# Kernel optimization log

Hardware: AMD Instinct MI355X
Metric: run time of the kernel (lower is better)

Reference implementation:

```python
import jax, jax.numpy as jnp
import numpy as np

N = 50000   # nodes
E = 800000  # edges
R = 2000    # relations
F = 128     # node_F / rel_F
DEPTH = 2
FD = F * (DEPTH + 1)  # 384
P = 64      # proxy rows
EPS = 1e-12


def setup_inputs() -> dict:
    key = jax.random.key(0)
    ks = jax.random.split(key, 16)
    inp = {
        'ent_emb': jax.random.normal(ks[0], (N, F), jnp.float32) * 0.05,
        'rel_emb': jax.random.normal(ks[1], (R, F), jnp.float32) * 0.05,
        'edge_src': jax.random.randint(ks[2], (E,), 0, N, jnp.int32),
        'edge_dst': jax.random.randint(ks[3], (E,), 0, N, jnp.int32),
        'edge_rel': jax.random.randint(ks[4], (E,), 0, R, jnp.int32),
        'attn_e': jax.random.normal(ks[5], (DEPTH, F, 1), jnp.float32) * 0.1,
        'gate_e': jax.random.normal(ks[6], (FD, FD), jnp.float32) * 0.05,
        'proxy_e': jax.random.normal(ks[7], (P, FD), jnp.float32) * 0.1,
        'bias_e': jnp.zeros((1, FD), jnp.float32),
        'attn_r': jax.random.normal(ks[8], (DEPTH, F, 1), jnp.float32) * 0.1,
        'gate_r': jax.random.normal(ks[9], (FD, FD), jnp.float32) * 0.05,
        'proxy_r': jax.random.normal(ks[10], (P, FD), jnp.float32) * 0.1,
        'bias_r': jnp.zeros((1, FD), jnp.float32),
    }
    return inp


def _l2norm(x, axis=-1):
    n = jnp.sqrt(jnp.sum(x * x, axis=axis, keepdims=True))
    return x / jnp.maximum(n, EPS)


def _dual(features, rel_emb, edge_src, edge_dst, edge_rel,
          attn_kernels, gate_kernel, proxy, bias):
    feats = jnp.tanh(features)            # [N, F]
    outs = [feats]
    for l in range(DEPTH):
        # per-edge relation feature (mean over relation set == gather here), L2-normalized
        rels_sum = _l2norm(rel_emb[edge_rel])          # [E, F]
        neighs = feats[edge_src]                       # [E, F]
        # Householder reflection of neighbor features across relation direction
        dot = jnp.sum(neighs * rels_sum, axis=1, keepdims=True)
        neighs = neighs - 2.0 * dot * rels_sum
        # edge_softmax normalized by dst
        att1 = jnp.squeeze(rels_sum @ attn_kernels[l], -1)   # [E]
        seg_max = jax.ops.segment_max(att1, edge_dst, num_segments=N)
        ex = jnp.exp(att1 - seg_max[edge_dst])
        seg_sum = jax.ops.segment_sum(ex, edge_dst, num_segments=N)
        att = ex / seg_sum[edge_dst]
        # weighted scatter-sum aggregation
        agg = jax.ops.segment_sum(neighs * att[:, None], edge_dst, num_segments=N)
        feats = jnp.tanh(agg)
        outs.append(feats)
    outputs = jnp.concatenate(outs, axis=1)            # [N, FD]
    proxy_att = jax.nn.softmax(_l2norm(outputs) @ _l2norm(proxy).T, axis=-1)  # [N, P]
    proxy_feature = outputs - proxy_att @ proxy
    gate = jax.nn.sigmoid(proxy_feature @ gate_kernel + bias)
    return gate * outputs + (1.0 - gate) * proxy_feature


def reference(ent_emb, rel_emb, edge_src, edge_dst, edge_rel,
              attn_e, gate_e, proxy_e, bias_e,
              attn_r, gate_r, proxy_r, bias_r):
    # initial features: mean of neighbor entity / relation embeddings per dst node
    deg = jax.ops.segment_sum(jnp.ones((E,), jnp.float32), edge_dst, num_segments=N)
    deg = jnp.maximum(deg, 1.0)[:, None]
    ent_feature = jax.ops.segment_sum(ent_emb[edge_src], edge_dst, num_segments=N) / deg
    rel_feature = jax.ops.segment_sum(rel_emb[edge_rel], edge_dst, num_segments=N) / deg
    out_ent = _dual(ent_feature, rel_emb, edge_src, edge_dst, edge_rel,
                    attn_e, gate_e, proxy_e, bias_e)
    out_rel = _dual(rel_feature, rel_emb, edge_src, edge_dst, edge_rel,
                    attn_r, gate_r, proxy_r, bias_r)
    return jnp.concatenate((out_ent, out_rel), axis=-1)  # [N, 2*FD]
```

## Files before the change

### kernel.cpp

```cpp
#include <hip/hip_runtime.h>
#include <math.h>


#define NN    50000
#define NE    800000
#define NR    2000
#define FF    128
#define FDIM  384
#define OD    768
#define PP    64
#define NEPS  1e-12f
#define NPB   32
#define FSTR  388
#define ASTR  68
#define NBLK  49

typedef unsigned int u32;
typedef unsigned short u16;
typedef __attribute__((ext_vector_type(8))) short bf16x8;
typedef __attribute__((ext_vector_type(4))) float f32x4;

__device__ int   g_rowptr[NN + 1];
__device__ int   g_cnt[NN];
__device__ int   g_bsum[64];
__device__ u32   g_csr[NE];
__device__ float g_relnorm[NR * FF];
__device__ float2 g_ew[2 * NR];
__device__ __attribute__((aligned(16))) u16 g_wt_hi[2 * FDIM * FDIM];
__device__ __attribute__((aligned(16))) u16 g_wt_lo[2 * FDIM * FDIM];
__device__ __attribute__((aligned(16))) u16 g_pxn_hi[2 * PP * FDIM];
__device__ __attribute__((aligned(16))) u16 g_pxn_lo[2 * PP * FDIM];
__device__ __attribute__((aligned(16))) u16 g_pxT_hi[2 * FDIM * PP];
__device__ __attribute__((aligned(16))) u16 g_pxT_lo[2 * FDIM * PP];

__device__ __forceinline__ float wsum64(float v) {
#pragma unroll
    for (int m = 32; m > 0; m >>= 1) v += __shfl_xor(v, m, 64);
    return v;
}
__device__ __forceinline__ float wmax64(float v) {
#pragma unroll
    for (int m = 32; m > 0; m >>= 1) v = fmaxf(v, __shfl_xor(v, m, 64));
    return v;
}
__device__ __forceinline__ void red16x2(float& a, float& b) {
#pragma unroll
    for (int m = 1; m < 16; m <<= 1) {
        float ta = __shfl_xor(a, m, 64);
        float tb = __shfl_xor(b, m, 64);
        a += ta; b += tb;
    }
}
__device__ __forceinline__ void xgr4(float4& v) {
#pragma unroll
    for (int mk = 16; mk < 64; mk <<= 1) {
        v.x += __shfl_xor(v.x, mk, 64);
        v.y += __shfl_xor(v.y, mk, 64);
        v.z += __shfl_xor(v.z, mk, 64);
        v.w += __shfl_xor(v.w, mk, 64);
    }
}
__device__ __forceinline__ void xgr1(float& v) {
#pragma unroll
    for (int mk = 16; mk < 64; mk <<= 1) v += __shfl_xor(v, mk, 64);
}

__device__ __forceinline__ u32 pack_bf(float f) {
    u32 x = __float_as_uint(f);
    u32 hr = (x + 0x7FFFu + ((x >> 16) & 1u)) & 0xFFFF0000u;
    float res = f - __uint_as_float(hr);
    u32 y = __float_as_uint(res);
    u32 lr = (y + 0x7FFFu + ((y >> 16) & 1u)) >> 16;
    return hr | lr;
}
__device__ __forceinline__ float unpack_bf(u32 pk) {
    return __uint_as_float(pk & 0xFFFF0000u) + __uint_as_float(pk << 16);
}

__device__ __forceinline__ void load_afrag(const u32* p, bf16x8& ah, bf16x8& al) {
    u32 q[8];
    *reinterpret_cast<float4*>(q)     = *reinterpret_cast<const float4*>(p);
    *reinterpret_cast<float4*>(q + 4) = *reinterpret_cast<const float4*>(p + 4);
    union { u32 u[4]; bf16x8 v; } H, L;
#pragma unroll
    for (int j = 0; j < 4; j++) {
        H.u[j] = __builtin_amdgcn_perm(q[2 * j + 1], q[2 * j], 0x07060302u);
        L.u[j] = __builtin_amdgcn_perm(q[2 * j + 1], q[2 * j], 0x05040100u);
    }
    ah = H.v; al = L.v;
}

__global__ __launch_bounds__(256) void k_zero() {
    int i = blockIdx.x * 256 + threadIdx.x;
    if (i < NN) g_cnt[i] = 0;
}

__global__ __launch_bounds__(256) void k_prep_rel(
    const float* __restrict__ rel_emb, const float* __restrict__ attn_e,
    const float* __restrict__ attn_r) {
    int wave = threadIdx.x >> 6, lane = threadIdx.x & 63;
    int r = blockIdx.x * 4 + wave;
    if (r >= NR) return;
    float2 v = *(const float2*)(rel_emb + r * FF + 2 * lane);
    float ss = wsum64(v.x * v.x + v.y * v.y);
    float inv = 1.f / fmaxf(sqrtf(ss), NEPS);
    float rn0 = v.x * inv, rn1 = v.y * inv;
    *(float2*)(g_relnorm + r * FF + 2 * lane) = make_float2(rn0, rn1);
#pragma unroll
    for (int t = 0; t < 4; t++) {
        const float* av = ((t < 2) ? attn_e : attn_r) + (t & 1) * FF + 2 * lane;
        float d = wsum64(rn0 * av[0] + rn1 * av[1]);
        if (lane == 0) ((float*)&g_ew[(t & 1) * NR + r])[t >> 1] = expf(d);
    }
}

__global__ __launch_bounds__(256) void k_prep_proxy(
    const float* __restrict__ proxy_e, const float* __restrict__ proxy_r) {
    int wave = threadIdx.x >> 6, lane = threadIdx.x & 63;
    int row = blockIdx.x * 4 + wave;
    if (row >= 2 * PP) return;
    int d = row >> 6, p = row & 63;
    const float* pr = ((d == 0) ? proxy_e : proxy_r) + p * FDIM;
    float v[6];
    float ss = 0.f;
#pragma unroll
    for (int j = 0; j < 6; j++) {
        v[j] = pr[lane + 64 * j];
        ss += v[j] * v[j];
    }
    ss = wsum64(ss);
    float inv = 1.f / fmaxf(sqrtf(ss), NEPS);
#pragma unroll
    for (int j = 0; j < 6; j++) {
        int k = lane + 64 * j;
        u32 pn = pack_bf(v[j] * inv);
        g_pxn_hi[(d * PP + p) * FDIM + k] = (u16)(pn >> 16);
        g_pxn_lo[(d * PP + p) * FDIM + k] = (u16)(pn & 0xFFFFu);
        u32 pt = pack_bf(v[j]);
        g_pxT_hi[(d * FDIM + k) * PP + p] = (u16)(pt >> 16);
        g_pxT_lo[(d * FDIM + k) * PP + p] = (u16)(pt & 0xFFFFu);
    }
}

__global__ __launch_bounds__(256) void k_prep_wt(
    const float* __restrict__ gate_e, const float* __restrict__ gate_r) {
    int idx = blockIdx.x * 256 + threadIdx.x;
    if (idx >= 2 * FDIM * FDIM) return;
    int d = idx / (FDIM * FDIM);
    int rem = idx - d * (FDIM * FDIM);
    int k = rem / FDIM;
    int f = rem - k * FDIM;
    float wv = (d ? gate_r : gate_e)[k * FDIM + f];
    u32 pk = pack_bf(wv);
    g_wt_hi[(d * FDIM + f) * FDIM + k] = (u16)(pk >> 16);
    g_wt_lo[(d * FDIM + f) * FDIM + k] = (u16)(pk & 0xFFFFu);
}

__global__ __launch_bounds__(256) void k_count(const int* __restrict__ dst) {
    int e = blockIdx.x * 256 + threadIdx.x;
    if (e < NE) atomicAdd(&g_cnt[dst[e]], 1);
}

__global__ __launch_bounds__(1024) void k_scan1() {
    __shared__ int s[1024];
    int b = blockIdx.x, tid = threadIdx.x;
    int i = b * 1024 + tid;
    int v = (i < NN) ? g_cnt[i] : 0;
    s[tid] = v;
    __syncthreads();
    for (int off = 1; off < 1024; off <<= 1) {
        int t = (tid >= off) ? s[tid - off] : 0;
        __syncthreads();
        s[tid] += t;
        __syncthreads();
    }
    if (i < NN) {
        g_rowptr[i] = s[tid] - v;
        g_cnt[i] = 0;
    }
    if (tid == 1023) g_bsum[b] = s[1023];
}
__global__ __launch_bounds__(64) void k_scan2() {
    int lane = threadIdx.x;
    int v = (lane < NBLK) ? g_bsum[lane] : 0;
#pragma unroll
    for (int off = 1; off < 64; off <<= 1) {
        int t = __shfl_up(v, off, 64);
        if (lane >= off) v += t;
    }
    if (lane < NBLK) g_bsum[lane] = v;
    if (lane == 0) g_rowptr[NN] = NE;
}
__global__ __launch_bounds__(1024) void k_scan3() {
    int b = blockIdx.x;
    if (b == 0) return;
    int i = b * 1024 + threadIdx.x;
    if (i < NN) g_rowptr[i] += g_bsum[b - 1];
}

__global__ __launch_bounds__(256) void k_fill(
    const int* __restrict__ src, const int* __restrict__ dst,
    const int* __restrict__ rel) {
    int e = blockIdx.x * 256 + threadIdx.x;
    if (e >= NE) return;
    int d = dst[e];
    int pos = atomicAdd(&g_cnt[d], 1);
    g_csr[g_rowptr[d] + pos] = ((u32)src[e] << 16) | (u32)rel[e];
}

__global__ __launch_bounds__(256) void k_init(
    const float* __restrict__ ent_emb, const float* __restrict__ rel_emb,
    float* __restrict__ out) {
    int wave = threadIdx.x >> 6, lane = threadIdx.x & 63;
    int n = blockIdx.x * 4 + wave;
    if (n >= NN) return;
    int g16 = lane >> 4, li = lane & 15;
    int s0 = g_rowptr[n], s1 = g_rowptr[n + 1];
    float4 aeA = {0,0,0,0}, aeB = {0,0,0,0}, arA = {0,0,0,0}, arB = {0,0,0,0};
    for (int idx = s0; idx < s1; idx += 4) {
        int e = idx + g16;
        if (e < s1) {
            u32 pk = g_csr[e];
            int s = (int)(pk >> 16), r = (int)(pk & 0xFFFFu);
            const float* up = ent_emb + (size_t)s * FF + 8 * li;
            const float* rp = rel_emb + (size_t)r * FF + 8 * li;
            float4 u0 = *(const float4*)up, u1 = *(const float4*)(up + 4);
            float4 r0 = *(const float4*)rp, r1 = *(const float4*)(rp + 4);
            aeA.x += u0.x; aeA.y += u0.y; aeA.z += u0.z; aeA.w += u0.w;
            aeB.x += u1.x; aeB.y += u1.y; aeB.z += u1.z; aeB.w += u1.w;
            arA.x += r0.x; arA.y += r0.y; arA.z += r0.z; arA.w += r0.w;
            arB.x += r1.x; arB.y += r1.y; arB.z += r1.z; arB.w += r1.w;
        }
    }
    xgr4(aeA); xgr4(aeB); xgr4(arA); xgr4(arB);
    float invd = 1.f / (float)max(s1 - s0, 1);
    if (g16 == 0) {
        float* oe = out + (size_t)n * OD + 8 * li;
        float* orp = out + (size_t)n * OD + FDIM + 8 * li;
        *(float4*)oe = make_float4(tanhf(aeA.x * invd), tanhf(aeA.y * invd),
                                   tanhf(aeA.z * invd), tanhf(aeA.w * invd));
        *(float4*)(oe + 4) = make_float4(tanhf(aeB.x * invd), tanhf(aeB.y * invd),
                                         tanhf(aeB.z * invd), tanhf(aeB.w * invd));
        *(float4*)orp = make_float4(tanhf(arA.x * invd), tanhf(arA.y * invd),
                                    tanhf(arA.z * invd), tanhf(arA.w * invd));
        *(float4*)(orp + 4) = make_float4(tanhf(arB.x * invd), tanhf(arB.y * invd),
                                          tanhf(arB.z * invd), tanhf(arB.w * invd));
    }
}

__global__ __launch_bounds__(256) void k_layer(float* buf, int layer) {
    int wave = threadIdx.x >> 6, lane = threadIdx.x & 63;
    int n = blockIdx.x * 4 + wave;
    if (n >= NN) return;
    int g16 = lane >> 4, li = lane & 15;
    int bi_e = layer * FF, bi_r = FDIM + layer * FF;
    const float2* ew = g_ew + layer * NR;
    int s0 = g_rowptr[n], s1 = g_rowptr[n + 1];
    float* oe = buf + (size_t)n * OD + bi_e + FF;
    float* orp = buf + (size_t)n * OD + bi_r + FF;
    if (s1 == s0) {
        if (g16 == 0) {
            *(float4*)(oe + 8 * li) = make_float4(0.f, 0.f, 0.f, 0.f);
            *(float4*)(oe + 8 * li + 4) = make_float4(0.f, 0.f, 0.f, 0.f);
            *(float4*)(orp + 8 * li) = make_float4(0.f, 0.f, 0.f, 0.f);
            *(float4*)(orp + 8 * li + 4) = make_float4(0.f, 0.f, 0.f, 0.f);
        }
        return;
    }
    float4 aeA = {0,0,0,0}, aeB = {0,0,0,0}, arA = {0,0,0,0}, arB = {0,0,0,0};
    float wse = 0.f, wsr = 0.f;
    for (int idx = s0; idx < s1; idx += 4) {
        int e = idx + g16;
        bool act = e < s1;
        u32 pk = g_csr[act ? e : s0];
        int s = (int)(pk >> 16), r = (int)(pk & 0xFFFFu);
        const float* hb = buf + (size_t)s * OD;
        float4 he0 = *(const float4*)(hb + bi_e + 8 * li);
        float4 he1 = *(const float4*)(hb + bi_e + 8 * li + 4);
        float4 hr0 = *(const float4*)(hb + bi_r + 8 * li);
        float4 hr1 = *(const float4*)(hb + bi_r + 8 * li + 4);
        const float* rp = g_relnorm + (size_t)r * FF + 8 * li;
        float4 rn0 = *(const float4*)rp;
        float4 rn1 = *(const float4*)(rp + 4);
        float de = he0.x * rn0.x + he0.y * rn0.y + he0.z * rn0.z + he0.w * rn0.w
                 + he1.x * rn1.x + he1.y * rn1.y + he1.z * rn1.z + he1.w * rn1.w;
        float dr = hr0.x * rn0.x + hr0.y * rn0.y + hr0.z * rn0.z + hr0.w * rn0.w
                 + hr1.x * rn1.x + hr1.y * rn1.y + hr1.z * rn1.z + hr1.w * rn1.w;
        red16x2(de, dr);
        float2 wv = act ? ew[r] : make_float2(0.f, 0.f);
        wse += wv.x; wsr += wv.y;
        float te = -2.f * de, tr = -2.f * dr;
        aeA.x = fmaf(wv.x, fmaf(te, rn0.x, he0.x), aeA.x);
        aeA.y = fmaf(wv.x, fmaf(te, rn0.y, he0.y), aeA.y);
        aeA.z = fmaf(wv.x, fmaf(te, rn0.z, he0.z), aeA.z);
        aeA.w = fmaf(wv.x, fmaf(te, rn0.w, he0.w), aeA.w);
        aeB.x = fmaf(wv.x, fmaf(te, rn1.x, he1.x), aeB.x);
        aeB.y = fmaf(wv.x, fmaf(te, rn1.y, he1.y), aeB.y);
        aeB.z = fmaf(wv.x, fmaf(te, rn1.z, he1.z), aeB.z);
        aeB.w = fmaf(wv.x, fmaf(te, rn1.w, he1.w), aeB.w);
        arA.x = fmaf(wv.y, fmaf(tr, rn0.x, hr0.x), arA.x);
        arA.y = fmaf(wv.y, fmaf(tr, rn0.y, hr0.y), arA.y);
        arA.z = fmaf(wv.y, fmaf(tr, rn0.z, hr0.z), arA.z);
        arA.w = fmaf(wv.y, fmaf(tr, rn0.w, hr0.w), arA.w);
        arB.x = fmaf(wv.y, fmaf(tr, rn1.x, hr1.x), arB.x);
        arB.y = fmaf(wv.y, fmaf(tr, rn1.y, hr1.y), arB.y);
        arB.z = fmaf(wv.y, fmaf(tr, rn1.z, hr1.z), arB.z);
        arB.w = fmaf(wv.y, fmaf(tr, rn1.w, hr1.w), arB.w);
    }
    xgr4(aeA); xgr4(aeB); xgr4(arA); xgr4(arB);
    xgr1(wse); xgr1(wsr);
    float ive = 1.f / wse, ivr = 1.f / wsr;
    if (g16 == 0) {
        *(float4*)(oe + 8 * li) = make_float4(tanhf(aeA.x * ive), tanhf(aeA.y * ive),
                                              tanhf(aeA.z * ive), tanhf(aeA.w * ive));
        *(float4*)(oe + 8 * li + 4) = make_float4(tanhf(aeB.x * ive), tanhf(aeB.y * ive),
                                                  tanhf(aeB.z * ive), tanhf(aeB.w * ive));
        *(float4*)(orp + 8 * li) = make_float4(tanhf(arA.x * ivr), tanhf(arA.y * ivr),
                                               tanhf(arA.z * ivr), tanhf(arA.w * ivr));
        *(float4*)(orp + 8 * li + 4) = make_float4(tanhf(arB.x * ivr), tanhf(arB.y * ivr),
                                                   tanhf(arB.z * ivr), tanhf(arB.w * ivr));
    }
}

__global__ __launch_bounds__(256, 2) void k_pg(
    float* out, const float* __restrict__ bias_e,
    const float* __restrict__ bias_r) {
    __shared__ __attribute__((aligned(16))) u32 o_pk[NPB * FSTR];
    __shared__ __attribute__((aligned(16))) u32 att_pk[NPB * ASTR];
    __shared__ float invn_s[NPB];
    int tid = threadIdx.x;
    int lane = tid & 63, w = tid >> 6;
    int c = lane & 15, kg = lane >> 4;
    int n0 = blockIdx.x * NPB, dual = blockIdx.y;
    int dual_off = dual * FDIM;
    const float* bias = dual ? bias_r : bias_e;
    const u16* wt_h = g_wt_hi + dual * (FDIM * FDIM);
    const u16* wt_l = g_wt_lo + dual * (FDIM * FDIM);
    const u16* pn_h = g_pxn_hi + dual * (PP * FDIM);
    const u16* pn_l = g_pxn_lo + dual * (PP * FDIM);
    const u16* pt_h = g_pxT_hi + dual * (FDIM * PP);
    const u16* pt_l = g_pxT_lo + dual * (FDIM * PP);

#pragma unroll
    for (int j = 0; j < 8; j++) {
        int n = w + 4 * j;
        int gn = n0 + n;
        float2 v[3];
        if (gn < NN) {
            const float* rp = out + (size_t)gn * OD + dual_off;
#pragma unroll
            for (int q = 0; q < 3; q++) v[q] = *(const float2*)(rp + 2 * (lane + 64 * q));
        } else {
            v[0] = v[1] = v[2] = make_float2(0.f, 0.f);
        }
        float ss = 0.f;
#pragma unroll
        for (int q = 0; q < 3; q++) ss += v[q].x * v[q].x + v[q].y * v[q].y;
        ss = wsum64(ss);
        if (lane == 0) invn_s[n] = 1.f / fmaxf(sqrtf(ss), NEPS);
#pragma unroll
        for (int q = 0; q < 3; q++) {
            uint2 pr;
            pr.x = pack_bf(v[q].x);
            pr.y = pack_bf(v[q].y);
            *(uint2*)(o_pk + n * FSTR + 2 * (lane + 64 * q)) = pr;
        }
    }
    __syncthreads();

    {
        f32x4 lacc[2] = {{0.f,0.f,0.f,0.f},{0.f,0.f,0.f,0.f}};
        const u16* bh_p = pn_h + (16 * w + c) * FDIM;
        const u16* bl_p = pn_l + (16 * w + c) * FDIM;
#pragma unroll 2
        for (int ks = 0; ks < 12; ks++) {
            int kb = 32 * ks + 8 * kg;
            bf16x8 bh = *(const bf16x8*)(bh_p + kb);
            bf16x8 bl = *(const bf16x8*)(bl_p + kb);
#pragma unroll
            for (int m = 0; m < 2; m++) {
                bf16x8 ah, al;
                load_afrag(o_pk + (16 * m + c) * FSTR + kb, ah, al);
                lacc[m] = __builtin_amdgcn_mfma_f32_16x16x32_bf16(ah, bh, lacc[m], 0, 0, 0);
                lacc[m] = __builtin_amdgcn_mfma_f32_16x16x32_bf16(al, bh, lacc[m], 0, 0, 0);
                lacc[m] = __builtin_amdgcn_mfma_f32_16x16x32_bf16(ah, bl, lacc[m], 0, 0, 0);
            }
        }
#pragma unroll
        for (int m = 0; m < 2; m++)
#pragma unroll
            for (int i = 0; i < 4; i++) {
                int n = 16 * m + 4 * kg + i;
                att_pk[n * ASTR + 16 * w + c] = __float_as_uint(lacc[m][i] * invn_s[n]);
            }
    }
    __syncthreads();

#pragma unroll
    for (int j = 0; j < 8; j++) {
        int n = w + 4 * j;
        float l = __uint_as_float(att_pk[n * ASTR + lane]);
        float mx = wmax64(l);
        float e = expf(l - mx);
        float s = wsum64(e);
        att_pk[n * ASTR + lane] = pack_bf(e / s);
    }
    __syncthreads();

    f32x4 pacc[2][6];
#pragma unroll
    for (int m = 0; m < 2; m++)
#pragma unroll
        for (int t = 0; t < 6; t++) pacc[m][t] = (f32x4){0.f, 0.f, 0.f, 0.f};
    {
        bf16x8 aah[2][2], aal[2][2];
#pragma unroll
        for (int m = 0; m < 2; m++) {
            load_afrag(att_pk + (16 * m + c) * ASTR + 8 * kg, aah[m][0], aal[m][0]);
            load_afrag(att_pk + (16 * m + c) * ASTR + 32 + 8 * kg, aah[m][1], aal[m][1]);
        }
#pragma unroll
        for (int t = 0; t < 6; t++) {
            int f = 96 * w + 16 * t + c;
            const u16* bh0 = pt_h + f * PP;
            const u16* bl0 = pt_l + f * PP;
            bf16x8 b0h = *(const bf16x8*)(bh0 + 8 * kg);
            bf16x8 b0l = *(const bf16x8*)(bl0 + 8 * kg);
            bf16x8 b1h = *(const bf16x8*)(bh0 + 32 + 8 * kg);
            bf16x8 b1l = *(const bf16x8*)(bl0 + 32 + 8 * kg);
#pragma unroll
            for (int m = 0; m < 2; m++) {
                pacc[m][t] = __builtin_amdgcn_mfma_f32_16x16x32_bf16(aah[m][0], b0h, pacc[m][t], 0, 0, 0);
                pacc[m][t] = __builtin_amdgcn_mfma_f32_16x16x32_bf16(aal[m][0], b0h, pacc[m][t], 0, 0, 0);
                pacc[m][t] = __builtin_amdgcn_mfma_f32_16x16x32_bf16(aah[m][0], b0l, pacc[m][t], 0, 0, 0);
                pacc[m][t] = __builtin_amdgcn_mfma_f32_16x16x32_bf16(aah[m][1], b1h, pacc[m][t], 0, 0, 0);
                pacc[m][t] = __builtin_amdgcn_mfma_f32_16x16x32_bf16(aal[m][1], b1h, pacc[m][t], 0, 0, 0);
                pacc[m][t] = __builtin_amdgcn_mfma_f32_16x16x32_bf16(aah[m][1], b1l, pacc[m][t], 0, 0, 0);
            }
        }
#pragma unroll
        for (int t = 0; t < 6; t++) {
            int f = 96 * w + 16 * t + c;
#pragma unroll
            for (int m = 0; m < 2; m++)
#pragma unroll
                for (int i = 0; i < 4; i++) {
                    int n = 16 * m + 4 * kg + i;
                    u32 pk = o_pk[n * FSTR + f];
                    o_pk[n * FSTR + f] = pack_bf(unpack_bf(pk) - pacc[m][t][i]);
                }
        }
    }
    __syncthreads();

    f32x4 gacc[2][6];
#pragma unroll
    for (int m = 0; m < 2; m++)
#pragma unroll
        for (int t = 0; t < 6; t++) gacc[m][t] = (f32x4){0.f, 0.f, 0.f, 0.f};
    {
        const u16* wtw_h = wt_h + (96 * w + c) * FDIM;
        const u16* wtw_l = wt_l + (96 * w + c) * FDIM;
#pragma unroll 2
        for (int ks = 0; ks < 12; ks++) {
            int kb = 32 * ks + 8 * kg;
            bf16x8 bhv[6], blv[6];
#pragma unroll
            for (int t = 0; t < 6; t++) {
                bhv[t] = *(const bf16x8*)(wtw_h + t * 16 * FDIM + kb);
                blv[t] = *(const bf16x8*)(wtw_l + t * 16 * FDIM + kb);
            }
            bf16x8 ah[2], al[2];
#pragma unroll
            for (int m = 0; m < 2; m++)
                load_afrag(o_pk + (16 * m + c) * FSTR + kb, ah[m], al[m]);
#pragma unroll
            for (int t = 0; t < 6; t++)
#pragma unroll
                for (int m = 0; m < 2; m++) {
                    gacc[m][t] = __builtin_amdgcn_mfma_f32_16x16x32_bf16(ah[m], bhv[t], gacc[m][t], 0, 0, 0);
                    gacc[m][t] = __builtin_amdgcn_mfma_f32_16x16x32_bf16(al[m], bhv[t], gacc[m][t], 0, 0, 0);
                    gacc[m][t] = __builtin_amdgcn_mfma_f32_16x16x32_bf16(ah[m], blv[t], gacc[m][t], 0, 0, 0);
                }
        }
    }

#pragma unroll
    for (int t = 0; t < 6; t++) {
        int fcol = 96 * w + 16 * t + c;
        float b = bias[fcol];
#pragma unroll
        for (int m = 0; m < 2; m++)
#pragma unroll
            for (int i = 0; i < 4; i++) {
                int n = 16 * m + 4 * kg + i;
                int gn = n0 + n;
                if (gn < NN) {
                    float lin = gacc[m][t][i] + b;
                    float gt = 1.f / (1.f + expf(-lin));
                    float pv = unpack_bf(o_pk[n * FSTR + fcol]);
                    float ov = pv + pacc[m][t][i];
                    out[(size_t)gn * OD + dual_off + fcol] = gt * ov + (1.f - gt) * pv;
                }
            }
    }
}

extern "C" void kernel_launch(void* const* d_in, const int* in_sizes, int n_in,
                              void* d_out, int out_size, void* d_ws, size_t ws_size,
                              hipStream_t stream) {
    const float* ent_emb = (const float*)d_in[0];
    const float* rel_emb = (const float*)d_in[1];
    const int* e_src     = (const int*)d_in[2];
    const int* e_dst     = (const int*)d_in[3];
    const int* e_rel     = (const int*)d_in[4];
    const float* attn_e  = (const float*)d_in[5];
    const float* gate_e  = (const float*)d_in[6];
    const float* proxy_e = (const float*)d_in[7];
    const float* bias_e  = (const float*)d_in[8];
    const float* attn_r  = (const float*)d_in[9];
    const float* gate_r  = (const float*)d_in[10];
    const float* proxy_r = (const float*)d_in[11];
    const float* bias_r  = (const float*)d_in[12];
    float* out = (float*)d_out;
    (void)d_ws; (void)ws_size; (void)in_sizes; (void)n_in; (void)out_size;

    k_zero<<<(NN + 255) / 256, 256, 0, stream>>>();
    k_prep_rel<<<NR / 4, 256, 0, stream>>>(rel_emb, attn_e, attn_r);
    k_prep_proxy<<<32, 256, 0, stream>>>(proxy_e, proxy_r);
    k_prep_wt<<<(2 * FDIM * FDIM + 255) / 256, 256, 0, stream>>>(gate_e, gate_r);
    k_count<<<(NE + 255) / 256, 256, 0, stream>>>(e_dst);
    k_scan1<<<NBLK, 1024, 0, stream>>>();
    k_scan2<<<1, 64, 0, stream>>>();
    k_scan3<<<NBLK, 1024, 0, stream>>>();
    k_fill<<<(NE + 255) / 256, 256, 0, stream>>>(e_src, e_dst, e_rel);
    k_init<<<NN / 4, 256, 0, stream>>>(ent_emb, rel_emb, out);
    k_layer<<<NN / 4, 256, 0, stream>>>(out, 0);
    k_layer<<<NN / 4, 256, 0, stream>>>(out, 1);
    k_pg<<<dim3((NN + NPB - 1) / NPB, 2), 256, 0, stream>>>(out, bias_e, bias_r);
}
```

Baseline: 1.017 ms.

## Gather neighbor features from compact fp16 copies and batch warp reductions

Adds fp16 shadow copies of the entity embeddings and of each layer's node features in a dense 256-wide layout. The init and layer kernels now gather from these copies instead of strided fp32 rows in the output buffer, which halves gather bytes and improves locality. The proxy-gate kernel batches its row-norm and softmax reductions across 8 rows and drops the softmax max-subtraction, adding ILP but risking overflow for large logits. fp16 gathers also lose precision in the Householder and aggregation math.

```diff
diff --git a/kernel.cpp b/kernel.cpp
--- a/kernel.cpp
+++ b/kernel.cpp
@@ -18,6 +18,7 @@
 typedef unsigned int u32;
 typedef unsigned short u16;
 typedef __attribute__((ext_vector_type(8))) short bf16x8;
+typedef __attribute__((ext_vector_type(8))) _Float16 f16x8;
 typedef __attribute__((ext_vector_type(4))) float f32x4;
 
 __device__ int   g_rowptr[NN + 1];
@@ -26,6 +27,8 @@
 __device__ u32   g_csr[NE];
 __device__ float g_relnorm[NR * FF];
 __device__ float2 g_ew[2 * NR];
+__device__ __attribute__((aligned(16))) _Float16 g_hh[2][NN][256];
+__device__ __attribute__((aligned(16))) _Float16 g_ent16[NN * FF];
 __device__ __attribute__((aligned(16))) u16 g_wt_hi[2 * FDIM * FDIM];
 __device__ __attribute__((aligned(16))) u16 g_wt_lo[2 * FDIM * FDIM];
 __device__ __attribute__((aligned(16))) u16 g_pxn_hi[2 * PP * FDIM];
@@ -38,11 +41,6 @@
     for (int m = 32; m > 0; m >>= 1) v += __shfl_xor(v, m, 64);
     return v;
 }
-__device__ __forceinline__ float wmax64(float v) {
-#pragma unroll
-    for (int m = 32; m > 0; m >>= 1) v = fmaxf(v, __shfl_xor(v, m, 64));
-    return v;
-}
 __device__ __forceinline__ void red16x2(float& a, float& b) {
 #pragma unroll
     for (int m = 1; m < 16; m <<= 1) {
@@ -50,19 +48,6 @@
         float tb = __shfl_xor(b, m, 64);
         a += ta; b += tb;
     }
-}
-__device__ __forceinline__ void xgr4(float4& v) {
-#pragma unroll
-    for (int mk = 16; mk < 64; mk <<= 1) {
-        v.x += __shfl_xor(v.x, mk, 64);
-        v.y += __shfl_xor(v.y, mk, 64);
-        v.z += __shfl_xor(v.z, mk, 64);
-        v.w += __shfl_xor(v.w, mk, 64);
-    }
-}
-__device__ __forceinline__ void xgr1(float& v) {
-#pragma unroll
-    for (int mk = 16; mk < 64; mk <<= 1) v += __shfl_xor(v, mk, 64);
 }
 
 __device__ __forceinline__ u32 pack_bf(float f) {
@@ -112,6 +97,17 @@
         float d = wsum64(rn0 * av[0] + rn1 * av[1]);
         if (lane == 0) ((float*)&g_ew[(t & 1) * NR + r])[t >> 1] = expf(d);
     }
+}
+
+__global__ __launch_bounds__(256) void k_prep_ent(const float* __restrict__ ent_emb) {
+    int i = (blockIdx.x * 256 + threadIdx.x) * 8;
+    if (i >= NN * FF) return;
+    float4 a = *(const float4*)(ent_emb + i);
+    float4 b = *(const float4*)(ent_emb + i + 4);
+    f16x8 h;
+    h[0] = (_Float16)a.x; h[1] = (_Float16)a.y; h[2] = (_Float16)a.z; h[3] = (_Float16)a.w;
+    h[4] = (_Float16)b.x; h[5] = (_Float16)b.y; h[6] = (_Float16)b.z; h[7] = (_Float16)b.w;
+    *(f16x8*)(g_ent16 + i) = h;
 }
 
 __global__ __launch_bounds__(256) void k_prep_proxy(
@@ -209,42 +205,58 @@
 }
 
 __global__ __launch_bounds__(256) void k_init(
-    const float* __restrict__ ent_emb, const float* __restrict__ rel_emb,
-    float* __restrict__ out) {
+    const float* __restrict__ rel_emb, float* __restrict__ out) {
     int wave = threadIdx.x >> 6, lane = threadIdx.x & 63;
     int n = blockIdx.x * 4 + wave;
     if (n >= NN) return;
     int g16 = lane >> 4, li = lane & 15;
     int s0 = g_rowptr[n], s1 = g_rowptr[n + 1];
-    float4 aeA = {0,0,0,0}, aeB = {0,0,0,0}, arA = {0,0,0,0}, arB = {0,0,0,0};
+    float ae[8], ar[8];
+#pragma unroll
+    for (int i = 0; i < 8; i++) { ae[i] = 0.f; ar[i] = 0.f; }
     for (int idx = s0; idx < s1; idx += 4) {
         int e = idx + g16;
         if (e < s1) {
             u32 pk = g_csr[e];
             int s = (int)(pk >> 16), r = (int)(pk & 0xFFFFu);
-            const float* up = ent_emb + (size_t)s * FF + 8 * li;
+            f16x8 ev = *(const f16x8*)(g_ent16 + (size_t)s * FF + 8 * li);
             const float* rp = rel_emb + (size_t)r * FF + 8 * li;
-            float4 u0 = *(const float4*)up, u1 = *(const float4*)(up + 4);
             float4 r0 = *(const float4*)rp, r1 = *(const float4*)(rp + 4);
-            aeA.x += u0.x; aeA.y += u0.y; aeA.z += u0.z; aeA.w += u0.w;
-            aeB.x += u1.x; aeB.y += u1.y; aeB.z += u1.z; aeB.w += u1.w;
-            arA.x += r0.x; arA.y += r0.y; arA.z += r0.z; arA.w += r0.w;
-            arB.x += r1.x; arB.y += r1.y; arB.z += r1.z; arB.w += r1.w;
-        }
-    }
-    xgr4(aeA); xgr4(aeB); xgr4(arA); xgr4(arB);
+            float rv[8] = {r0.x, r0.y, r0.z, r0.w, r1.x, r1.y, r1.z, r1.w};
+#pragma unroll
+            for (int i = 0; i < 8; i++) {
+                ae[i] += (float)ev[i];
+                ar[i] += rv[i];
+            }
+        }
+    }
+#pragma unroll
+    for (int mk = 16; mk < 64; mk <<= 1)
+#pragma unroll
+        for (int i = 0; i < 8; i++) {
+            ae[i] += __shfl_xor(ae[i], mk, 64);
+            ar[i] += __shfl_xor(ar[i], mk, 64);
+        }
     float invd = 1.f / (float)max(s1 - s0, 1);
     if (g16 == 0) {
+        float fe[8], fr[8];
+#pragma unroll
+        for (int i = 0; i < 8; i++) {
+            fe[i] = tanhf(ae[i] * invd);
+            fr[i] = tanhf(ar[i] * invd);
+        }
         float* oe = out + (size_t)n * OD + 8 * li;
         float* orp = out + (size_t)n * OD + FDIM + 8 * li;
-        *(float4*)oe = make_float4(tanhf(aeA.x * invd), tanhf(aeA.y * invd),
-                                   tanhf(aeA.z * invd), tanhf(aeA.w * invd));
-        *(float4*)(oe + 4) = make_float4(tanhf(aeB.x * invd), tanhf(aeB.y * invd),
-                                         tanhf(aeB.z * invd), tanhf(aeB.w * invd));
-        *(float4*)orp = make_float4(tanhf(arA.x * invd), tanhf(arA.y * invd),
-                                    tanhf(arA.z * invd), tanhf(arA.w * invd));
-        *(float4*)(orp + 4) = make_float4(tanhf(arB.x * invd), tanhf(arB.y * invd),
-                                          tanhf(arB.z * invd), tanhf(arB.w * invd));
+        *(float4*)oe = make_float4(fe[0], fe[1], fe[2], fe[3]);
+        *(float4*)(oe + 4) = make_float4(fe[4], fe[5], fe[6], fe[7]);
+        *(float4*)orp = make_float4(fr[0], fr[1], fr[2], fr[3]);
+        *(float4*)(orp + 4) = make_float4(fr[4], fr[5], fr[6], fr[7]);
+        _Float16* hh = &g_hh[0][n][0];
+        f16x8 he, hr;
+#pragma unroll
+        for (int i = 0; i < 8; i++) { he[i] = (_Float16)fe[i]; hr[i] = (_Float16)fr[i]; }
+        *(f16x8*)(hh + 8 * li) = he;
+        *(f16x8*)(hh + 128 + 8 * li) = hr;
     }
 }
 
@@ -253,72 +265,95 @@
     int n = blockIdx.x * 4 + wave;
     if (n >= NN) return;
     int g16 = lane >> 4, li = lane & 15;
-    int bi_e = layer * FF, bi_r = FDIM + layer * FF;
+    int bo_e = (layer + 1) * FF;
+    int bo_r = FDIM + (layer + 1) * FF;
     const float2* ew = g_ew + layer * NR;
+    const _Float16* hs = &g_hh[layer][0][0];
     int s0 = g_rowptr[n], s1 = g_rowptr[n + 1];
-    float* oe = buf + (size_t)n * OD + bi_e + FF;
-    float* orp = buf + (size_t)n * OD + bi_r + FF;
     if (s1 == s0) {
         if (g16 == 0) {
-            *(float4*)(oe + 8 * li) = make_float4(0.f, 0.f, 0.f, 0.f);
-            *(float4*)(oe + 8 * li + 4) = make_float4(0.f, 0.f, 0.f, 0.f);
-            *(float4*)(orp + 8 * li) = make_float4(0.f, 0.f, 0.f, 0.f);
-            *(float4*)(orp + 8 * li + 4) = make_float4(0.f, 0.f, 0.f, 0.f);
+            float* oe = buf + (size_t)n * OD + bo_e + 8 * li;
+            float* orp = buf + (size_t)n * OD + bo_r + 8 * li;
+            *(float4*)oe = make_float4(0.f, 0.f, 0.f, 0.f);
+            *(float4*)(oe + 4) = make_float4(0.f, 0.f, 0.f, 0.f);
+            *(float4*)orp = make_float4(0.f, 0.f, 0.f, 0.f);
+            *(float4*)(orp + 4) = make_float4(0.f, 0.f, 0.f, 0.f);
+            if (layer == 0) {
+                _Float16* hh = &g_hh[1][n][0];
+                f16x8 z = (f16x8)(_Float16)0.f;
+                *(f16x8*)(hh + 8 * li) = z;
+                *(f16x8*)(hh + 128 + 8 * li) = z;
+            }
         }
         return;
     }
-    float4 aeA = {0,0,0,0}, aeB = {0,0,0,0}, arA = {0,0,0,0}, arB = {0,0,0,0};
+    float ae[8], ar[8];
+#pragma unroll
+    for (int i = 0; i < 8; i++) { ae[i] = 0.f; ar[i] = 0.f; }
     float wse = 0.f, wsr = 0.f;
     for (int idx = s0; idx < s1; idx += 4) {
         int e = idx + g16;
         bool act = e < s1;
         u32 pk = g_csr[act ? e : s0];
         int s = (int)(pk >> 16), r = (int)(pk & 0xFFFFu);
-        const float* hb = buf + (size_t)s * OD;
-        float4 he0 = *(const float4*)(hb + bi_e + 8 * li);
-        float4 he1 = *(const float4*)(hb + bi_e + 8 * li + 4);
-        float4 hr0 = *(const float4*)(hb + bi_r + 8 * li);
-        float4 hr1 = *(const float4*)(hb + bi_r + 8 * li + 4);
+        const _Float16* hrow = hs + (size_t)s * 256;
+        f16x8 hev = *(const f16x8*)(hrow + 8 * li);
+        f16x8 hrv = *(const f16x8*)(hrow + 128 + 8 * li);
         const float* rp = g_relnorm + (size_t)r * FF + 8 * li;
         float4 rn0 = *(const float4*)rp;
         float4 rn1 = *(const float4*)(rp + 4);
-        float de = he0.x * rn0.x + he0.y * rn0.y + he0.z * rn0.z + he0.w * rn0.w
-                 + he1.x * rn1.x + he1.y * rn1.y + he1.z * rn1.z + he1.w * rn1.w;
-        float dr = hr0.x * rn0.x + hr0.y * rn0.y + hr0.z * rn0.z + hr0.w * rn0.w
-                 + hr1.x * rn1.x + hr1.y * rn1.y + hr1.z * rn1.z + hr1.w * rn1.w;
+        float rnv[8] = {rn0.x, rn0.y, rn0.z, rn0.w, rn1.x, rn1.y, rn1.z, rn1.w};
+        float he[8], hr[8];
+#pragma unroll
+        for (int i = 0; i < 8; i++) { he[i] = (float)hev[i]; hr[i] = (float)hrv[i]; }
+        float de = 0.f, dr = 0.f;
+#pragma unroll
+        for (int i = 0; i < 8; i++) {
+            de = fmaf(he[i], rnv[i], de);
+            dr = fmaf(hr[i], rnv[i], dr);
+        }
         red16x2(de, dr);
         float2 wv = act ? ew[r] : make_float2(0.f, 0.f);
         wse += wv.x; wsr += wv.y;
         float te = -2.f * de, tr = -2.f * dr;
-        aeA.x = fmaf(wv.x, fmaf(te, rn0.x, he0.x), aeA.x);
-        aeA.y = fmaf(wv.x, fmaf(te, rn0.y, he0.y), aeA.y);
-        aeA.z = fmaf(wv.x, fmaf(te, rn0.z, he0.z), aeA.z);
-        aeA.w = fmaf(wv.x, fmaf(te, rn0.w, he0.w), aeA.w);
-        aeB.x = fmaf(wv.x, fmaf(te, rn1.x, he1.x), aeB.x);
-        aeB.y = fmaf(wv.x, fmaf(te, rn1.y, he1.y), aeB.y);
-        aeB.z = fmaf(wv.x, fmaf(te, rn1.z, he1.z), aeB.z);
-        aeB.w = fmaf(wv.x, fmaf(te, rn1.w, he1.w), aeB.w);
-        arA.x = fmaf(wv.y, fmaf(tr, rn0.x, hr0.x), arA.x);
-        arA.y = fmaf(wv.y, fmaf(tr, rn0.y, hr0.y), arA.y);
-        arA.z = fmaf(wv.y, fmaf(tr, rn0.z, hr0.z), arA.z);
-        arA.w = fmaf(wv.y, fmaf(tr, rn0.w, hr0.w), arA.w);
-        arB.x = fmaf(wv.y, fmaf(tr, rn1.x, hr1.x), arB.x);
-        arB.y = fmaf(wv.y, fmaf(tr, rn1.y, hr1.y), arB.y);
-        arB.z = fmaf(wv.y, fmaf(tr, rn1.z, hr1.z), arB.z);
-        arB.w = fmaf(wv.y, fmaf(tr, rn1.w, hr1.w), arB.w);
-    }
-    xgr4(aeA); xgr4(aeB); xgr4(arA); xgr4(arB);
-    xgr1(wse); xgr1(wsr);
+#pragma unroll
+        for (int i = 0; i < 8; i++) {
+            ae[i] = fmaf(wv.x, fmaf(te, rnv[i], he[i]), ae[i]);
+            ar[i] = fmaf(wv.y, fmaf(tr, rnv[i], hr[i]), ar[i]);
+        }
+    }
+#pragma unroll
+    for (int mk = 16; mk < 64; mk <<= 1) {
+#pragma unroll
+        for (int i = 0; i < 8; i++) {
+            ae[i] += __shfl_xor(ae[i], mk, 64);
+            ar[i] += __shfl_xor(ar[i], mk, 64);
+        }
+        wse += __shfl_xor(wse, mk, 64);
+        wsr += __shfl_xor(wsr, mk, 64);
+    }
     float ive = 1.f / wse, ivr = 1.f / wsr;
     if (g16 == 0) {
-        *(float4*)(oe + 8 * li) = make_float4(tanhf(aeA.x * ive), tanhf(aeA.y * ive),
-                                              tanhf(aeA.z * ive), tanhf(aeA.w * ive));
-        *(float4*)(oe + 8 * li + 4) = make_float4(tanhf(aeB.x * ive), tanhf(aeB.y * ive),
-                                                  tanhf(aeB.z * ive), tanhf(aeB.w * ive));
-        *(float4*)(orp + 8 * li) = make_float4(tanhf(arA.x * ivr), tanhf(arA.y * ivr),
-                                               tanhf(arA.z * ivr), tanhf(arA.w * ivr));
-        *(float4*)(orp + 8 * li + 4) = make_float4(tanhf(arB.x * ivr), tanhf(arB.y * ivr),
-                                                   tanhf(arB.z * ivr), tanhf(arB.w * ivr));
+        float fe[8], fr[8];
+#pragma unroll
+        for (int i = 0; i < 8; i++) {
+            fe[i] = tanhf(ae[i] * ive);
+            fr[i] = tanhf(ar[i] * ivr);
+        }
+        float* oe = buf + (size_t)n * OD + bo_e + 8 * li;
+        float* orp = buf + (size_t)n * OD + bo_r + 8 * li;
+        *(float4*)oe = make_float4(fe[0], fe[1], fe[2], fe[3]);
+        *(float4*)(oe + 4) = make_float4(fe[4], fe[5], fe[6], fe[7]);
+        *(float4*)orp = make_float4(fr[0], fr[1], fr[2], fr[3]);
+        *(float4*)(orp + 4) = make_float4(fr[4], fr[5], fr[6], fr[7]);
+        if (layer == 0) {
+            _Float16* hh = &g_hh[1][n][0];
+            f16x8 he16, hr16;
+#pragma unroll
+            for (int i = 0; i < 8; i++) { he16[i] = (_Float16)fe[i]; hr16[i] = (_Float16)fr[i]; }
+            *(f16x8*)(hh + 8 * li) = he16;
+            *(f16x8*)(hh + 128 + 8 * li) = hr16;
+        }
     }
 }
 
@@ -341,29 +376,39 @@
     const u16* pt_h = g_pxT_hi + dual * (FDIM * PP);
     const u16* pt_l = g_pxT_lo + dual * (FDIM * PP);
 
-#pragma unroll
-    for (int j = 0; j < 8; j++) {
-        int n = w + 4 * j;
-        int gn = n0 + n;
-        float2 v[3];
-        if (gn < NN) {
-            const float* rp = out + (size_t)gn * OD + dual_off;
-#pragma unroll
-            for (int q = 0; q < 3; q++) v[q] = *(const float2*)(rp + 2 * (lane + 64 * q));
-        } else {
-            v[0] = v[1] = v[2] = make_float2(0.f, 0.f);
-        }
-        float ss = 0.f;
-#pragma unroll
-        for (int q = 0; q < 3; q++) ss += v[q].x * v[q].x + v[q].y * v[q].y;
-        ss = wsum64(ss);
-        if (lane == 0) invn_s[n] = 1.f / fmaxf(sqrtf(ss), NEPS);
-#pragma unroll
-        for (int q = 0; q < 3; q++) {
-            uint2 pr;
-            pr.x = pack_bf(v[q].x);
-            pr.y = pack_bf(v[q].y);
-            *(uint2*)(o_pk + n * FSTR + 2 * (lane + 64 * q)) = pr;
+    {
+        float2 v[8][3];
+        float ss[8];
+#pragma unroll
+        for (int j = 0; j < 8; j++) {
+            int n = w + 4 * j;
+            int gn = n0 + n;
+            if (gn < NN) {
+                const float* rp = out + (size_t)gn * OD + dual_off;
+#pragma unroll
+                for (int q = 0; q < 3; q++) v[j][q] = *(const float2*)(rp + 2 * (lane + 64 * q));
+            } else {
+                v[j][0] = v[j][1] = v[j][2] = make_float2(0.f, 0.f);
+            }
+            ss[j] = v[j][0].x * v[j][0].x + v[j][0].y * v[j][0].y
+                  + v[j][1].x * v[j][1].x + v[j][1].y * v[j][1].y
+                  + v[j][2].x * v[j][2].x + v[j][2].y * v[j][2].y;
+        }
+#pragma unroll
+        for (int m = 32; m > 0; m >>= 1)
+#pragma unroll
+            for (int j = 0; j < 8; j++) ss[j] += __shfl_xor(ss[j], m, 64);
+#pragma unroll
+        for (int j = 0; j < 8; j++) {
+            int n = w + 4 * j;
+            if (lane == 0) invn_s[n] = 1.f / fmaxf(sqrtf(ss[j]), NEPS);
+#pragma unroll
+            for (int q = 0; q < 3; q++) {
+                uint2 pr;
+                pr.x = pack_bf(v[j][q].x);
+                pr.y = pack_bf(v[j][q].y);
+                *(uint2*)(o_pk + n * FSTR + 2 * (lane + 64 * q)) = pr;
+            }
         }
     }
     __syncthreads();
@@ -396,14 +441,23 @@
     }
     __syncthreads();
 
-#pragma unroll
-    for (int j = 0; j < 8; j++) {
-        int n = w + 4 * j;
-        float l = __uint_as_float(att_pk[n * ASTR + lane]);
-        float mx = wmax64(l);
-        float e = expf(l - mx);
-        float s = wsum64(e);
-        att_pk[n * ASTR + lane] = pack_bf(e / s);
+    {
+        float ev[8], sv[8];
+#pragma unroll
+        for (int j = 0; j < 8; j++) {
+            int n = w + 4 * j;
+            ev[j] = expf(__uint_as_float(att_pk[n * ASTR + lane]));
+            sv[j] = ev[j];
+        }
+#pragma unroll
+        for (int m = 32; m > 0; m >>= 1)
+#pragma unroll
+            for (int j = 0; j < 8; j++) sv[j] += __shfl_xor(sv[j], m, 64);
+#pragma unroll
+        for (int j = 0; j < 8; j++) {
+            int n = w + 4 * j;
+            att_pk[n * ASTR + lane] = pack_bf(ev[j] / sv[j]);
+        }
     }
     __syncthreads();
 
@@ -527,6 +581,7 @@
 
     k_zero<<<(NN + 255) / 256, 256, 0, stream>>>();
     k_prep_rel<<<NR / 4, 256, 0, stream>>>(rel_emb, attn_e, attn_r);
+    k_prep_ent<<<(NN * FF / 8 + 255) / 256, 256, 0, stream>>>(ent_emb);
     k_prep_proxy<<<32, 256, 0, stream>>>(proxy_e, proxy_r);
     k_prep_wt<<<(2 * FDIM * FDIM + 255) / 256, 256, 0, stream>>>(gate_e, gate_r);
     k_count<<<(NE + 255) / 256, 256, 0, stream>>>(e_dst);
@@ -534,7 +589,7 @@
     k_scan2<<<1, 64, 0, stream>>>();
     k_scan3<<<NBLK, 1024, 0, stream>>>();
     k_fill<<<(NE + 255) / 256, 256, 0, stream>>>(e_src, e_dst, e_rel);
-    k_init<<<NN / 4, 256, 0, stream>>>(ent_emb, rel_emb, out);
+    k_init<<<NN / 4, 256, 0, stream>>>(rel_emb, out);
     k_layer<<<NN / 4, 256, 0, stream>>>(out, 0);
     k_layer<<<NN / 4, 256, 0, stream>>>(out, 1);
     k_pg<<<dim3((NN + NPB - 1) / NPB, 2), 256, 0, stream>>>(out, bias_e, bias_r);
```

Result: faster. 866.1 us (-14.9%).
